# Optimization experiments

Measured on AMD Instinct MI355X. Metric: run time of the kernel, lower is better.

Reference implementation:

```python
import jax, jax.numpy as jnp
import numpy as np

B, T, D, H = 2, 2048, 1024, 16
HS = D // H  # head_size = 64


def setup_inputs() -> dict:
    key = jax.random.key(0)
    ks = jax.random.split(key, 8)
    scale = D ** -0.5
    q = jax.random.normal(ks[0], (B, T, D), dtype=jnp.float32)
    k = jax.random.normal(ks[1], (B, T, D), dtype=jnp.float32)
    v = jax.random.normal(ks[2], (B, T, D), dtype=jnp.float32)
    # per-head projection weights (no bias), stacked over heads: [H, D, HS]
    Wq = jax.random.normal(ks[3], (H, D, HS), dtype=jnp.float32) * scale
    Wk = jax.random.normal(ks[4], (H, D, HS), dtype=jnp.float32) * scale
    Wv = jax.random.normal(ks[5], (H, D, HS), dtype=jnp.float32) * scale
    # output projection Linear(H*HS, D) with bias
    Wo = jax.random.normal(ks[6], (D, D), dtype=jnp.float32) * scale
    bo = jnp.zeros((D,), dtype=jnp.float32)
    # causal mask, broadcastable to [B, T, T]; mask==0 -> -inf
    mask = jnp.tril(jnp.ones((T, T), dtype=bool))[None]
    return {"q": q, "k": k, "v": v, "Wq": Wq, "Wk": Wk, "Wv": Wv,
            "Wo": Wo, "bo": bo, "mask": mask}


def reference(q, k, v, Wq, Wk, Wv, Wo, bo, mask):
    # Batched equivalent of the per-head loop: project all heads at once.
    Q = jnp.einsum('btc,hcd->bhtd', q, Wq)  # [B,H,T,HS]
    K = jnp.einsum('btc,hcd->bhtd', k, Wk)
    V = jnp.einsum('btc,hcd->bhtd', v, Wv)
    wei = jnp.einsum('bhtd,bhsd->bhts', Q, K) * (HS ** -0.5)  # [B,H,T,T]
    wei = jnp.where(mask[:, None, :, :], wei, jnp.float32(-jnp.inf))
    attn = jax.nn.softmax(wei, axis=-1)  # dropout is identity in eval
    out = jnp.einsum('bhts,bhsd->bhtd', attn, V)
    out = out.transpose(0, 2, 1, 3).reshape(B, T, D)  # concat heads
    return out @ Wo + bo
```

## Files before the change

### kernel.cpp

```cpp
#include <hip/hip_runtime.h>
#include <hip/hip_bf16.h>
#include <math.h>

#define BB 2
#define TT 2048
#define DM 1024
#define NH 16
#define HS 64
#define MM (BB*TT)

typedef __attribute__((ext_vector_type(8))) short s16x8;
typedef __attribute__((ext_vector_type(4))) float f32x4;

#define MFMA16(a,b,c) __builtin_amdgcn_mfma_f32_16x16x32_bf16((a),(b),(c),0,0,0)

__device__ inline unsigned short f2bf(float f) {
    union { float f; unsigned u; } x; x.f = f;
    unsigned r = x.u + 0x7fff + ((x.u >> 16) & 1);
    return (unsigned short)(r >> 16);
}
__device__ inline unsigned short f2bfr(float f) {
    union { float f; unsigned u; } x; x.f = f;
    return (unsigned short)((x.u + 0x8000u) >> 16);
}

__device__ __forceinline__ void gload16(const void* g, void* l) {
    __builtin_amdgcn_global_load_lds(
        (const __attribute__((address_space(1))) unsigned int*)g,
        (__attribute__((address_space(3))) unsigned int*)l, 16, 0, 0);
}

__global__ __launch_bounds__(256) void cvt_w_kernel(
    const float* __restrict__ W0, const float* __restrict__ W1,
    const float* __restrict__ W2, unsigned short* __restrict__ dst, int wo_mode)
{
    __shared__ __align__(16) short Tt[64 * 72];
    const int t = threadIdx.x;
    const int d0 = blockIdx.x * 64;
    const int h  = blockIdx.y;
    const int z  = blockIdx.z;
    const float* W = (z == 0) ? W0 : (z == 1) ? W1 : W2;
    unsigned short* dz = dst + (size_t)z * DM * DM;

    const int hs4 = (t & 15) * 4;
    const int dl0 = t >> 4;
    #pragma unroll
    for (int it = 0; it < 4; ++it) {
        int dl = it * 16 + dl0;
        const float* src = wo_mode
            ? &W[(size_t)(d0 + dl) * DM + h * 64 + hs4]
            : &W[(size_t)h * DM * HS + (size_t)(d0 + dl) * HS + hs4];
        float4 vv = *(const float4*)src;
        Tt[(hs4 + 0) * 72 + dl] = (short)f2bf(vv.x);
        Tt[(hs4 + 1) * 72 + dl] = (short)f2bf(vv.y);
        Tt[(hs4 + 2) * 72 + dl] = (short)f2bf(vv.z);
        Tt[(hs4 + 3) * 72 + dl] = (short)f2bf(vv.w);
    }
    __syncthreads();
    int hs = t >> 2, doff = (t & 3) * 16;
    s16x8 r0 = *(s16x8*)&Tt[hs * 72 + doff];
    s16x8 r1 = *(s16x8*)&Tt[hs * 72 + doff + 8];
    unsigned short* op = dz + (size_t)(h * 64 + hs) * DM + d0 + doff;
    *(s16x8*)op = r0;
    *(s16x8*)(op + 8) = r1;
}

__global__ __launch_bounds__(512) void proj_gemm_kernel(
    const float* __restrict__ q, const float* __restrict__ k,
    const float* __restrict__ v, const unsigned short* __restrict__ Wt,
    unsigned short* __restrict__ Qb, unsigned short* __restrict__ Kb,
    unsigned short* __restrict__ Vt)
{
    __shared__ __align__(16) unsigned short As[2][128 * 32];
    __shared__ __align__(16) unsigned short Bs[2][128 * 32];

    const int tid = threadIdx.x;
    const int l = tid & 63, w = tid >> 6;
    const int wr = w >> 2, wc = w & 3;
    const int g = l >> 4, r16 = l & 15;

    const int bid = blockIdx.x;
    const int xcd = bid & 7, u = bid >> 3;
    const int z = u >> 5, vv = u & 31;
    const int n0 = (vv >> 2) * 128;
    const int m0 = (xcd * 4 + (vv & 3)) * 128;

    const float* x = (z == 0) ? q : (z == 1) ? k : v;
    const unsigned short* Wz = Wt + (size_t)z * DM * DM;

    const int ar = tid >> 2, aq = tid & 3;
    const float* axp = x + (size_t)(m0 + ar) * DM + aq * 8;
    const int axr = (ar >> 1) & 3;
    const int awof = ar * 32 + ((aq ^ axr) * 8);

    const int brow = tid >> 2, bgl = tid & 3;
    const unsigned short* bS = Wz + (size_t)(n0 + brow) * DM
                             + ((bgl ^ ((brow >> 1) & 3)) * 8);
    const int bDof = tid * 8;

    int aoff[4], boff[2];
    #pragma unroll
    for (int i = 0; i < 4; ++i) {
        int row = wr * 64 + i * 16 + r16;
        aoff[i] = row * 32 + ((g ^ ((row >> 1) & 3)) * 8);
    }
    #pragma unroll
    for (int c = 0; c < 2; ++c) {
        int row = wc * 32 + c * 16 + r16;
        boff[c] = row * 32 + ((g ^ ((row >> 1) & 3)) * 8);
    }

    f32x4 acc[4][2];
    #pragma unroll
    for (int i = 0; i < 4; ++i)
        #pragma unroll
        for (int c = 0; c < 2; ++c)
            #pragma unroll
            for (int j = 0; j < 4; ++j) acc[i][c][j] = 0.0f;

    float4 al0, al1;

    #define PLOADA(k0_) do {                                             \
        const float* ap = axp + (k0_);                                   \
        al0 = *(const float4*)(ap);                                      \
        al1 = *(const float4*)(ap + 4);                                  \
    } while (0)

    #define GLOADB(buf, k0_) gload16(bS + (k0_), &Bs[(buf)][bDof])

    #define PSTORE(buf) do {                                             \
        union { s16x8 v; __hip_bfloat162 h[4]; } c0;                     \
        c0.h[0] = __float22bfloat162_rn(make_float2(al0.x, al0.y));      \
        c0.h[1] = __float22bfloat162_rn(make_float2(al0.z, al0.w));      \
        c0.h[2] = __float22bfloat162_rn(make_float2(al1.x, al1.y));      \
        c0.h[3] = __float22bfloat162_rn(make_float2(al1.z, al1.w));      \
        *(s16x8*)&As[(buf)][awof] = c0.v;                                \
    } while (0)

    #define PCOMPUTE(buf) do {                                           \
        s16x8 af[4], bf[2];                                              \
        _Pragma("unroll")                                                \
        for (int i = 0; i < 4; ++i) af[i] = *(const s16x8*)&As[(buf)][aoff[i]]; \
        _Pragma("unroll")                                                \
        for (int c = 0; c < 2; ++c) bf[c] = *(const s16x8*)&Bs[(buf)][boff[c]]; \
        _Pragma("unroll")                                                \
        for (int i = 0; i < 4; ++i)                                      \
            _Pragma("unroll")                                            \
            for (int c = 0; c < 2; ++c)                                  \
                acc[i][c] = MFMA16(af[i], bf[c], acc[i][c]);             \
    } while (0)

    PLOADA(0);
    GLOADB(0, 0);
    PSTORE(0);
    for (int t = 0; t < 31; ++t) {
        const int cur = t & 1;
        PLOADA((t + 1) * 32);
        GLOADB(cur ^ 1, (t + 1) * 32);
        asm volatile("s_waitcnt vmcnt(3) lgkmcnt(0)" ::: "memory");
        __builtin_amdgcn_sched_barrier(0);
        __builtin_amdgcn_s_barrier();
        PCOMPUTE(cur);
        PSTORE(cur ^ 1);
        __builtin_amdgcn_s_barrier();
    }
    asm volatile("s_waitcnt vmcnt(0) lgkmcnt(0)" ::: "memory");
    __builtin_amdgcn_sched_barrier(0);
    __builtin_amdgcn_s_barrier();
    PCOMPUTE(1);
    #undef PLOADA
    #undef GLOADB
    #undef PSTORE
    #undef PCOMPUTE

    const int h = (n0 >> 6) + (wc >> 1);
    const int hsb = (wc & 1) * 32;
    if (z != 2) {
        unsigned short* dst = (z == 0) ? Qb : Kb;
        const float sc = (z == 0) ? 0.18033688011112042f : 1.0f;
        #pragma unroll
        for (int i = 0; i < 4; ++i)
            #pragma unroll
            for (int j = 0; j < 4; ++j) {
                int row = m0 + wr * 64 + i * 16 + g * 4 + j;
                int bb = row >> 11, tt = row & (TT - 1);
                size_t rb = (((size_t)(bb * NH + h)) * TT + tt) * HS;
                #pragma unroll
                for (int c = 0; c < 2; ++c)
                    dst[rb + hsb + c * 16 + r16] = f2bf(acc[i][c][j] * sc);
            }
    } else {
        #pragma unroll
        for (int i = 0; i < 4; ++i) {
            int row0 = m0 + wr * 64 + i * 16 + g * 4;
            int bb = row0 >> 11, tt0 = row0 & (TT - 1);
            #pragma unroll
            for (int c = 0; c < 2; ++c) {
                int hs = hsb + c * 16 + r16;
                union { unsigned long long u; unsigned short s[4]; } pk;
                #pragma unroll
                for (int j = 0; j < 4; ++j) pk.s[j] = f2bf(acc[i][c][j]);
                *(unsigned long long*)&Vt[(((size_t)(bb * NH + h)) * HS + hs) * TT + tt0] = pk.u;
            }
        }
    }
}

__global__ __launch_bounds__(512) void out_gemm_kernel(
    const unsigned short* __restrict__ Ob, const unsigned short* __restrict__ Wot,
    const float* __restrict__ bo, float* __restrict__ out)
{
    __shared__ __align__(16) unsigned short As2[2][128 * 32];
    __shared__ __align__(16) unsigned short Bs2[2][128 * 32];

    const int tid = threadIdx.x;
    const int l = tid & 63, w = tid >> 6;
    const int wr = w >> 2, wc = w & 3;
    const int g = l >> 4, r16 = l & 15;

    const int bid = blockIdx.x;
    const int xcd = bid & 7, u = bid >> 3;
    const int n0 = (u >> 2) * 128;
    const int m0 = (xcd * 4 + (u & 3)) * 128;

    const int srow = tid >> 2, sgl = tid & 3;
    const int scol = ((sgl ^ ((srow >> 1) & 3)) * 8);
    const unsigned short* aS = Ob + (size_t)(m0 + srow) * DM + scol;
    const unsigned short* bS = Wot + (size_t)(n0 + srow) * DM + scol;
    const int sDof = tid * 8;

    int aoff[4], boff[2];
    #pragma unroll
    for (int i = 0; i < 4; ++i) {
        int row = wr * 64 + i * 16 + r16;
        aoff[i] = row * 32 + ((g ^ ((row >> 1) & 3)) * 8);
    }
    #pragma unroll
    for (int c = 0; c < 2; ++c) {
        int row = wc * 32 + c * 16 + r16;
        boff[c] = row * 32 + ((g ^ ((row >> 1) & 3)) * 8);
    }

    f32x4 acc[4][2];
    #pragma unroll
    for (int i = 0; i < 4; ++i)
        #pragma unroll
        for (int c = 0; c < 2; ++c)
            #pragma unroll
            for (int j = 0; j < 4; ++j) acc[i][c][j] = 0.0f;

    #define OSTAGE(buf, k0_) do {                                        \
        gload16(aS + (k0_), &As2[(buf)][sDof]);                          \
        gload16(bS + (k0_), &Bs2[(buf)][sDof]);                          \
    } while (0)

    #define OCOMPUTE(buf) do {                                           \
        s16x8 af[4], bf[2];                                              \
        _Pragma("unroll")                                                \
        for (int i = 0; i < 4; ++i) af[i] = *(const s16x8*)&As2[(buf)][aoff[i]]; \
        _Pragma("unroll")                                                \
        for (int c = 0; c < 2; ++c) bf[c] = *(const s16x8*)&Bs2[(buf)][boff[c]]; \
        _Pragma("unroll")                                                \
        for (int i = 0; i < 4; ++i)                                      \
            _Pragma("unroll")                                            \
            for (int c = 0; c < 2; ++c)                                  \
                acc[i][c] = MFMA16(af[i], bf[c], acc[i][c]);             \
    } while (0)

    OSTAGE(0, 0);
    for (int t = 0; t < 31; ++t) {
        OSTAGE((t + 1) & 1, (t + 1) * 32);
        asm volatile("s_waitcnt vmcnt(2)" ::: "memory");
        __builtin_amdgcn_sched_barrier(0);
        __builtin_amdgcn_s_barrier();
        OCOMPUTE(t & 1);
        __builtin_amdgcn_s_barrier();
    }
    asm volatile("s_waitcnt vmcnt(0)" ::: "memory");
    __builtin_amdgcn_sched_barrier(0);
    __builtin_amdgcn_s_barrier();
    OCOMPUTE(1);
    #undef OSTAGE
    #undef OCOMPUTE

    #pragma unroll
    for (int i = 0; i < 4; ++i)
        #pragma unroll
        for (int j = 0; j < 4; ++j) {
            int row = m0 + wr * 64 + i * 16 + g * 4 + j;
            #pragma unroll
            for (int c = 0; c < 2; ++c) {
                int col = n0 + wc * 32 + c * 16 + r16;
                out[(size_t)row * DM + col] = acc[i][c][j] + bo[col];
            }
        }
}

template<bool MASKED>
__device__ __forceinline__ void ftile7(
    int kv0, int t0, int r16, int g,
    const unsigned short* __restrict__ Kl,
    const unsigned short* __restrict__ Vl,
    short* __restrict__ Pw,
    const s16x8 (&qf)[2],
    float& l_run, f32x4 (&o)[4])
{
    const int rs = r16 & 7;
    float pe[4][4];
    #pragma unroll
    for (int c = 0; c < 4; ++c) {
        if (!MASKED || (kv0 + c * 16 <= t0 + 15)) {
            f32x4 s0;
            #pragma unroll
            for (int j = 0; j < 4; ++j) s0[j] = 0.0f;
            const int base = (c * 16 + r16) * 64;
            s16x8 kf0 = *(const s16x8*)&Kl[base + ((g ^ rs) * 8)];
            s16x8 kf1 = *(const s16x8*)&Kl[base + (((4 + g) ^ rs) * 8)];
            s0 = MFMA16(kf0, qf[0], s0);
            s0 = MFMA16(kf1, qf[1], s0);
            #pragma unroll
            for (int j = 0; j < 4; ++j) {
                float e = __builtin_amdgcn_exp2f(s0[j] - 16.0f);
                if (MASKED)
                    e = (kv0 + c * 16 + g * 4 + j <= t0 + r16) ? e : 0.0f;
                pe[c][j] = e;
                l_run += e;
            }
        } else {
            #pragma unroll
            for (int j = 0; j < 4; ++j) pe[c][j] = 0.0f;
        }
    }

    #pragma unroll
    for (int c = 0; c < 2; ++c) {
        union { unsigned long long u; unsigned short s[4]; } pk;
        #pragma unroll
        for (int j = 0; j < 4; ++j) pk.s[j] = f2bfr(pe[c][j]);
        *(unsigned long long*)&Pw[r16 * 36 + c * 16 + g * 4] = pk.u;
    }
    {
        s16x8 pb = *(const s16x8*)&Pw[r16 * 36 + g * 8];
        #pragma unroll
        for (int c = 0; c < 4; ++c) {
            s16x8 vf = *(const s16x8*)&Vl[(c * 16 + r16) * 64 + ((g ^ rs) * 8)];
            o[c] = MFMA16(vf, pb, o[c]);
        }
    }
    if (!MASKED || (kv0 + 32 <= t0 + 15)) {
        #pragma unroll
        for (int c = 0; c < 2; ++c) {
            union { unsigned long long u; unsigned short s[4]; } pk;
            #pragma unroll
            for (int j = 0; j < 4; ++j) pk.s[j] = f2bfr(pe[2 + c][j]);
            *(unsigned long long*)&Pw[r16 * 36 + c * 16 + g * 4] = pk.u;
        }
        s16x8 pb = *(const s16x8*)&Pw[r16 * 36 + g * 8];
        #pragma unroll
        for (int c = 0; c < 4; ++c) {
            s16x8 vf = *(const s16x8*)&Vl[(c * 16 + r16) * 64 + (((4 + g) ^ rs) * 8)];
            o[c] = MFMA16(vf, pb, o[c]);
        }
    }
}

__global__ __launch_bounds__(512) void flash8_kernel(
    const unsigned short* __restrict__ Qb,
    const unsigned short* __restrict__ Kb,
    const unsigned short* __restrict__ Vt,
    unsigned short* __restrict__ Ob)
{
    __shared__ __align__(16) unsigned short Kls[2][4096];
    __shared__ __align__(16) unsigned short Vls[2][4096];
    __shared__ __align__(16) short Pl[8][576];

    const int tid = threadIdx.x;
    const int l = tid & 63, w = tid >> 6;
    const int r16 = l & 15, g = l >> 4;

    const int bid = blockIdx.x;
    const int bh = bid & 31;
    const int jj = bid >> 5;
    const int qc = (jj < 8) ? (15 - jj) : (jj - 8);
    const int numt = 2 * qc + 2;
    const int b = bh >> 4, h = bh & 15;

    const unsigned short* Qp = Qb + (size_t)bh * TT * HS;
    const unsigned short* Kp = Kb + (size_t)bh * TT * HS;
    const unsigned short* Vp = Vt + (size_t)bh * HS * TT;
    unsigned short* Op = Ob + (size_t)b * TT * DM + h * HS;
    short* Pw = Pl[w];

    const int t0 = qc * 128 + w * 16;

    const int srow = tid >> 3, c8 = tid & 7;
    const unsigned short* kS = Kp + srow * HS + ((c8 ^ (srow & 7)) * 8);
    const unsigned short* vS = Vp + (size_t)srow * TT + ((c8 ^ (srow & 7)) * 8);
    const int d0 = tid * 8;

    s16x8 qf[2];
    #pragma unroll
    for (int s = 0; s < 2; ++s)
        qf[s] = *(const s16x8*)(Qp + (size_t)(t0 + r16) * HS + s * 32 + g * 8);

    float l_run = 0.0f;
    f32x4 o[4];
    #pragma unroll
    for (int c = 0; c < 4; ++c)
        #pragma unroll
        for (int j = 0; j < 4; ++j) o[c][j] = 0.0f;

    #define STAGE(buf, kv0_) do {                                   \
        gload16(kS + (size_t)(kv0_) * HS, &Kls[(buf)][d0]);         \
        gload16(vS + (kv0_), &Vls[(buf)][d0]);                      \
    } while (0)

    #define FTILE(kv0_, buf_) do {                                  \
        if ((kv0_) + 64 <= t0 + 1)                                  \
            ftile7<false>((kv0_), t0, r16, g, &Kls[(buf_)][0],      \
                          &Vls[(buf_)][0], Pw, qf, l_run, o);       \
        else if ((kv0_) <= t0 + 15)                                 \
            ftile7<true>((kv0_), t0, r16, g, &Kls[(buf_)][0],       \
                         &Vls[(buf_)][0], Pw, qf, l_run, o);        \
    } while (0)

    STAGE(0, 0);
    for (int t = 0; t < numt - 1; ++t) {
        STAGE((t + 1) & 1, (t + 1) * 64);
        asm volatile("s_waitcnt vmcnt(2)" ::: "memory");
        __builtin_amdgcn_sched_barrier(0);
        __builtin_amdgcn_s_barrier();
        FTILE(t * 64, t & 1);
        __builtin_amdgcn_s_barrier();
    }
    asm volatile("s_waitcnt vmcnt(0)" ::: "memory");
    __builtin_amdgcn_sched_barrier(0);
    __builtin_amdgcn_s_barrier();
    FTILE((numt - 1) * 64, (numt - 1) & 1);
    #undef STAGE
    #undef FTILE

    float ls = l_run;
    ls += __shfl_xor(ls, 16);
    ls += __shfl_xor(ls, 32);
    const float inv = 1.0f / ls;
    unsigned short* rp = Op + (size_t)(t0 + r16) * DM;
    #pragma unroll
    for (int c = 0; c < 4; ++c) {
        union { unsigned long long u; unsigned short s[4]; } pk;
        #pragma unroll
        for (int j = 0; j < 4; ++j) pk.s[j] = f2bfr(o[c][j] * inv);
        *(unsigned long long*)&rp[c * 16 + g * 4] = pk.u;
    }
}

extern "C" void kernel_launch(void* const* d_in, const int* in_sizes, int n_in,
                              void* d_out, int out_size, void* d_ws, size_t ws_size,
                              hipStream_t stream) {
    const float* q  = (const float*)d_in[0];
    const float* k  = (const float*)d_in[1];
    const float* v  = (const float*)d_in[2];
    const float* Wq = (const float*)d_in[3];
    const float* Wk = (const float*)d_in[4];
    const float* Wv = (const float*)d_in[5];
    const float* Wo = (const float*)d_in[6];
    const float* bo = (const float*)d_in[7];
    float* out = (float*)d_out;

    const size_t QKV_ELEMS = (size_t)BB * NH * TT * HS;
    unsigned short* Qb = (unsigned short*)d_ws;
    unsigned short* Kb = Qb + QKV_ELEMS;
    unsigned short* Vt = Kb + QKV_ELEMS;
    unsigned short* R4 = Vt + QKV_ELEMS;
    unsigned short* Wt = R4;
    unsigned short* Ob = R4;
    unsigned short* Wot = Qb;

    cvt_w_kernel<<<dim3(16, 16, 3), 256, 0, stream>>>(Wq, Wk, Wv, Wt, 0);
    proj_gemm_kernel<<<dim3(768), 512, 0, stream>>>(q, k, v, Wt, Qb, Kb, Vt);
    flash8_kernel<<<dim3(512), 512, 0, stream>>>(Qb, Kb, Vt, Ob);
    cvt_w_kernel<<<dim3(16, 16, 1), 256, 0, stream>>>(Wo, Wo, Wo, Wot, 1);
    out_gemm_kernel<<<dim3(256), 512, 0, stream>>>(Ob, Wot, bo, out);
}
```

Measured before the change: 125.1 us.

## Pre-convert activations to bf16 and use direct LDS loads in projection GEMM

```diff
diff --git a/kernel.cpp b/kernel.cpp
--- a/kernel.cpp
+++ b/kernel.cpp
@@ -65,9 +65,26 @@
     *(s16x8*)(op + 8) = r1;
 }
 
-__global__ __launch_bounds__(512) void proj_gemm_kernel(
+__global__ __launch_bounds__(256) void cvt_x_kernel(
     const float* __restrict__ q, const float* __restrict__ k,
-    const float* __restrict__ v, const unsigned short* __restrict__ Wt,
+    const float* __restrict__ v, unsigned short* __restrict__ xb)
+{
+    const int z = blockIdx.z;
+    const float* x = (z == 0) ? q : (z == 1) ? k : v;
+    unsigned short* d = xb + (size_t)z * MM * DM;
+    const size_t i = ((size_t)blockIdx.x * 256 + threadIdx.x) * 8;
+    float4 a0 = *(const float4*)&x[i];
+    float4 a1 = *(const float4*)&x[i + 4];
+    union { s16x8 v; __hip_bfloat162 h[4]; } cv;
+    cv.h[0] = __float22bfloat162_rn(make_float2(a0.x, a0.y));
+    cv.h[1] = __float22bfloat162_rn(make_float2(a0.z, a0.w));
+    cv.h[2] = __float22bfloat162_rn(make_float2(a1.x, a1.y));
+    cv.h[3] = __float22bfloat162_rn(make_float2(a1.z, a1.w));
+    *(s16x8*)&d[i] = cv.v;
+}
+
+__global__ __launch_bounds__(256) void proj_gemm_kernel(
+    const unsigned short* __restrict__ xb, const unsigned short* __restrict__ Wt,
     unsigned short* __restrict__ Qb, unsigned short* __restrict__ Kb,
     unsigned short* __restrict__ Vt)
 {
@@ -76,7 +93,7 @@
 
     const int tid = threadIdx.x;
     const int l = tid & 63, w = tid >> 6;
-    const int wr = w >> 2, wc = w & 3;
+    const int wr = w >> 1, wc = w & 1;
     const int g = l >> 4, r16 = l & 15;
 
     const int bid = blockIdx.x;
@@ -85,96 +102,79 @@
     const int n0 = (vv >> 2) * 128;
     const int m0 = (xcd * 4 + (vv & 3)) * 128;
 
-    const float* x = (z == 0) ? q : (z == 1) ? k : v;
+    const unsigned short* Az = xb + (size_t)z * MM * DM;
     const unsigned short* Wz = Wt + (size_t)z * DM * DM;
 
-    const int ar = tid >> 2, aq = tid & 3;
-    const float* axp = x + (size_t)(m0 + ar) * DM + aq * 8;
-    const int axr = (ar >> 1) & 3;
-    const int awof = ar * 32 + ((aq ^ axr) * 8);
-
-    const int brow = tid >> 2, bgl = tid & 3;
-    const unsigned short* bS = Wz + (size_t)(n0 + brow) * DM
-                             + ((bgl ^ ((brow >> 1) & 3)) * 8);
-    const int bDof = tid * 8;
-
-    int aoff[4], boff[2];
+    const unsigned short* aS[2]; const unsigned short* bS[2];
+    int sDof[2];
+    #pragma unroll
+    for (int p = 0; p < 2; ++p) {
+        int qid = p * 256 + tid;
+        int row = qid >> 2, gl = qid & 3;
+        int col = ((gl ^ ((row >> 1) & 3)) * 8);
+        aS[p] = Az + (size_t)(m0 + row) * DM + col;
+        bS[p] = Wz + (size_t)(n0 + row) * DM + col;
+        sDof[p] = qid * 8;
+    }
+
+    int aoff[4], boff[4];
     #pragma unroll
     for (int i = 0; i < 4; ++i) {
         int row = wr * 64 + i * 16 + r16;
         aoff[i] = row * 32 + ((g ^ ((row >> 1) & 3)) * 8);
     }
     #pragma unroll
-    for (int c = 0; c < 2; ++c) {
-        int row = wc * 32 + c * 16 + r16;
+    for (int c = 0; c < 4; ++c) {
+        int row = wc * 64 + c * 16 + r16;
         boff[c] = row * 32 + ((g ^ ((row >> 1) & 3)) * 8);
     }
 
-    f32x4 acc[4][2];
+    f32x4 acc[4][4];
     #pragma unroll
     for (int i = 0; i < 4; ++i)
         #pragma unroll
-        for (int c = 0; c < 2; ++c)
+        for (int c = 0; c < 4; ++c)
             #pragma unroll
             for (int j = 0; j < 4; ++j) acc[i][c][j] = 0.0f;
 
-    float4 al0, al1;
-
-    #define PLOADA(k0_) do {                                             \
-        const float* ap = axp + (k0_);                                   \
-        al0 = *(const float4*)(ap);                                      \
-        al1 = *(const float4*)(ap + 4);                                  \
-    } while (0)
-
-    #define GLOADB(buf, k0_) gload16(bS + (k0_), &Bs[(buf)][bDof])
-
-    #define PSTORE(buf) do {                                             \
-        union { s16x8 v; __hip_bfloat162 h[4]; } c0;                     \
-        c0.h[0] = __float22bfloat162_rn(make_float2(al0.x, al0.y));      \
-        c0.h[1] = __float22bfloat162_rn(make_float2(al0.z, al0.w));      \
-        c0.h[2] = __float22bfloat162_rn(make_float2(al1.x, al1.y));      \
-        c0.h[3] = __float22bfloat162_rn(make_float2(al1.z, al1.w));      \
-        *(s16x8*)&As[(buf)][awof] = c0.v;                                \
+    #define PSTAGE(buf, k0_) do {                                        \
+        _Pragma("unroll")                                                \
+        for (int p = 0; p < 2; ++p) {                                    \
+            gload16(aS[p] + (k0_), &As[(buf)][sDof[p]]);                 \
+            gload16(bS[p] + (k0_), &Bs[(buf)][sDof[p]]);                 \
+        }                                                                \
     } while (0)
 
     #define PCOMPUTE(buf) do {                                           \
-        s16x8 af[4], bf[2];                                              \
+        s16x8 af[4], bf[4];                                              \
         _Pragma("unroll")                                                \
         for (int i = 0; i < 4; ++i) af[i] = *(const s16x8*)&As[(buf)][aoff[i]]; \
         _Pragma("unroll")                                                \
-        for (int c = 0; c < 2; ++c) bf[c] = *(const s16x8*)&Bs[(buf)][boff[c]]; \
+        for (int c = 0; c < 4; ++c) bf[c] = *(const s16x8*)&Bs[(buf)][boff[c]]; \
         _Pragma("unroll")                                                \
         for (int i = 0; i < 4; ++i)                                      \
             _Pragma("unroll")                                            \
-            for (int c = 0; c < 2; ++c)                                  \
+            for (int c = 0; c < 4; ++c)                                  \
                 acc[i][c] = MFMA16(af[i], bf[c], acc[i][c]);             \
     } while (0)
 
-    PLOADA(0);
-    GLOADB(0, 0);
-    PSTORE(0);
+    PSTAGE(0, 0);
     for (int t = 0; t < 31; ++t) {
-        const int cur = t & 1;
-        PLOADA((t + 1) * 32);
-        GLOADB(cur ^ 1, (t + 1) * 32);
-        asm volatile("s_waitcnt vmcnt(3) lgkmcnt(0)" ::: "memory");
+        PSTAGE((t + 1) & 1, (t + 1) * 32);
+        asm volatile("s_waitcnt vmcnt(4)" ::: "memory");
         __builtin_amdgcn_sched_barrier(0);
         __builtin_amdgcn_s_barrier();
-        PCOMPUTE(cur);
-        PSTORE(cur ^ 1);
-        __builtin_amdgcn_s_barrier();
-    }
-    asm volatile("s_waitcnt vmcnt(0) lgkmcnt(0)" ::: "memory");
+        PCOMPUTE(t & 1);
+        __builtin_amdgcn_s_barrier();
+    }
+    asm volatile("s_waitcnt vmcnt(0)" ::: "memory");
     __builtin_amdgcn_sched_barrier(0);
     __builtin_amdgcn_s_barrier();
     PCOMPUTE(1);
-    #undef PLOADA
-    #undef GLOADB
-    #undef PSTORE
+    #undef PSTAGE
     #undef PCOMPUTE
 
-    const int h = (n0 >> 6) + (wc >> 1);
-    const int hsb = (wc & 1) * 32;
+    const int h = (n0 >> 6) + wc;
     if (z != 2) {
         unsigned short* dst = (z == 0) ? Qb : Kb;
         const float sc = (z == 0) ? 0.18033688011112042f : 1.0f;
@@ -186,8 +186,8 @@
                 int bb = row >> 11, tt = row & (TT - 1);
                 size_t rb = (((size_t)(bb * NH + h)) * TT + tt) * HS;
                 #pragma unroll
-                for (int c = 0; c < 2; ++c)
-                    dst[rb + hsb + c * 16 + r16] = f2bf(acc[i][c][j] * sc);
+                for (int c = 0; c < 4; ++c)
+                    dst[rb + c * 16 + r16] = f2bf(acc[i][c][j] * sc);
             }
     } else {
         #pragma unroll
@@ -195,8 +195,8 @@
             int row0 = m0 + wr * 64 + i * 16 + g * 4;
             int bb = row0 >> 11, tt0 = row0 & (TT - 1);
             #pragma unroll
-            for (int c = 0; c < 2; ++c) {
-                int hs = hsb + c * 16 + r16;
+            for (int c = 0; c < 4; ++c) {
+                int hs = c * 16 + r16;
                 union { unsigned long long u; unsigned short s[4]; } pk;
                 #pragma unroll
                 for (int j = 0; j < 4; ++j) pk.s[j] = f2bf(acc[i][c][j]);
@@ -475,9 +475,11 @@
     unsigned short* Wt = R4;
     unsigned short* Ob = R4;
     unsigned short* Wot = Qb;
+    unsigned short* xb = R4 + QKV_ELEMS;
 
     cvt_w_kernel<<<dim3(16, 16, 3), 256, 0, stream>>>(Wq, Wk, Wv, Wt, 0);
-    proj_gemm_kernel<<<dim3(768), 512, 0, stream>>>(q, k, v, Wt, Qb, Kb, Vt);
+    cvt_x_kernel<<<dim3(2048, 1, 3), 256, 0, stream>>>(q, k, v, xb);
+    proj_gemm_kernel<<<dim3(768), 256, 0, stream>>>(xb, Wt, Qb, Kb, Vt);
     flash8_kernel<<<dim3(512), 512, 0, stream>>>(Qb, Kb, Vt, Ob);
     cvt_w_kernel<<<dim3(16, 16, 1), 256, 0, stream>>>(Wo, Wo, Wo, Wot, 1);
     out_gemm_kernel<<<dim3(256), 512, 0, stream>>>(Ob, Wot, bo, out);
```

Result: slower. 132.5 us (+5.9%).
